# Kernel tuning notes

Hardware: AMD Instinct MI355X
Metric: run time of the kernel (lower is better)

The kernel has to match this reference:

```python
import jax, jax.numpy as jnp
import numpy as np

N, E, G = 8192, 65536, 16          # atoms, edges, graphs in batch
NUM_ELEM, C, NB = 10, 64, 8        # elements, hidden channels, bessel basis
LMAX, NLAYERS = 3, 2
LM = (LMAX + 1) ** 2               # 16 spherical-harmonic components
R_MAX, P_CUT = 5.0, 5
EPS = 1e-9


def spherical_harmonics(u):
    # u: [E,3] unit vectors -> real spherical harmonics l<=3, [E,16]
    x, y, z = u[:, 0], u[:, 1], u[:, 2]
    x2, y2, z2 = x * x, y * y, z * z
    sh = [
        jnp.full_like(x, 0.28209479177387814),
        0.4886025119029199 * y, 0.4886025119029199 * z, 0.4886025119029199 * x,
        1.0925484305920792 * x * y, 1.0925484305920792 * y * z,
        0.31539156525252005 * (3.0 * z2 - 1.0),
        1.0925484305920792 * x * z, 0.5462742152960396 * (x2 - y2),
        0.5900435899266435 * y * (3.0 * x2 - y2), 2.890611442640554 * x * y * z,
        0.4570457994644658 * y * (5.0 * z2 - 1.0),
        0.3731763325901154 * z * (5.0 * z2 - 3.0),
        0.4570457994644658 * x * (5.0 * z2 - 1.0),
        1.445305721320277 * z * (x2 - y2),
        0.5900435899266435 * x * (x2 - 3.0 * y2),
    ]
    return jnp.stack(sh, axis=-1)


def radial_embedding(r):
    # Bessel radial basis with polynomial envelope cutoff -> [E, NB]
    u = r / R_MAX
    p = float(P_CUT)
    cut = (1.0 - 0.5 * (p + 1.0) * (p + 2.0) * u ** P_CUT
           + p * (p + 2.0) * u ** (P_CUT + 1)
           - 0.5 * p * (p + 1.0) * u ** (P_CUT + 2))
    cut = jnp.where(u < 1.0, cut, 0.0)
    n = jnp.arange(1, NB + 1, dtype=r.dtype)
    bessel = jnp.sqrt(2.0 / R_MAX) * jnp.sin(n[None, :] * jnp.pi * u[:, None]) \
             / jnp.maximum(r, EPS)[:, None]
    return bessel * cut[:, None]


def setup_inputs() -> dict:
    key = jax.random.key(0)
    ks = jax.random.split(key, 10)
    positions = jax.random.uniform(ks[0], (N, 3), jnp.float32) * 10.0
    elems = jax.random.randint(ks[1], (N,), 0, NUM_ELEM)
    node_attrs = jax.nn.one_hot(elems, NUM_ELEM, dtype=jnp.float32)
    edge_index = jax.random.randint(ks[2], (2, E), 0, N).astype(jnp.int32)
    shifts = jnp.zeros((E, 3), jnp.float32)
    batch = jnp.sort(jax.random.randint(ks[3], (N,), 0, G)).astype(jnp.int32)
    W_embed = jax.random.normal(ks[4], (NUM_ELEM, C), jnp.float32) / np.sqrt(NUM_ELEM)
    atomic_energies_w = jnp.arange(-1.0, -(NUM_ELEM + 1.0), -1.0, dtype=jnp.float32)
    W_rad = jax.random.normal(ks[5], (NLAYERS, NB, C), jnp.float32) / np.sqrt(NB)
    W_prod = jax.random.normal(ks[6], (NLAYERS, NUM_ELEM, (LMAX + 1) * C, C),
                               jnp.float32) / np.sqrt((LMAX + 1) * C)
    w_read = jax.random.normal(ks[7], (C,), jnp.float32) / np.sqrt(C)
    return {"positions": positions, "node_attrs": node_attrs, "shifts": shifts,
            "W_embed": W_embed, "atomic_energies_w": atomic_energies_w,
            "W_rad": W_rad, "W_prod": W_prod, "w_read": w_read,
            "edge_index": edge_index, "batch": batch}


def _energy(positions, node_attrs, shifts, W_embed, atomic_energies_w,
            W_rad, W_prod, w_read, edge_index, batch):
    snd, rcv = edge_index[0], edge_index[1]
    vec = positions[rcv] - positions[snd] + shifts            # [E,3]
    length = jnp.sqrt(jnp.sum(vec * vec, axis=-1) + EPS)      # [E]
    Y = spherical_harmonics(vec / length[:, None])            # [E,LM]
    R = radial_embedding(length)                              # [E,NB]

    e0 = jax.ops.segment_sum(node_attrs @ atomic_energies_w, batch, num_segments=G)
    h = node_attrs @ W_embed                                  # [N,C]

    for layer in range(NLAYERS):
        w = R @ W_rad[layer]                                  # [E,C] radial weights
        msg = (w * h[snd])[:, None, :] * Y[:, :, None]        # [E,LM,C] tensor product
        A = jax.ops.segment_sum(msg, rcv, num_segments=N)     # [N,LM,C] atomic basis
        A2 = A * A
        # invariant (rotation-invariant) contraction: sum over m within each l
        B = jnp.concatenate(
            [A2[:, l * l:(l + 1) * (l + 1), :].sum(axis=1) for l in range(LMAX + 1)],
            axis=-1)                                          # [N,(LMAX+1)*C]
        # element-dependent product-basis mixing
        h = jnp.einsum('nf,efc,ne->nc', B, W_prod[layer], node_attrs)

    node_e = h @ w_read                                       # [N]
    inter_e = jax.ops.segment_sum(node_e, batch, num_segments=G)
    return e0 + inter_e                                       # [G]


def reference(positions, node_attrs, shifts, W_embed, atomic_energies_w,
              W_rad, W_prod, w_read, edge_index, batch):
    energy = _energy(positions, node_attrs, shifts, W_embed, atomic_energies_w,
                     W_rad, W_prod, w_read, edge_index, batch)
    forces = -jax.grad(
        lambda p: _energy(p, node_attrs, shifts, W_embed, atomic_energies_w,
                          W_rad, W_prod, w_read, edge_index, batch).sum()
    )(positions)
    return energy, forces
```

## Files before the change

kernel.cpp:

```cpp
#include <hip/hip_runtime.h>
#include <math.h>

#define NN 8192
#define NE 65536
#define NG 16
#define NEL 10
#define CC 64
#define NLM 16
#define MAXST 32
#define PI_F 3.14159265358979f

__device__ __forceinline__ int lm_l(int lm) {
    return (lm == 0) ? 0 : (lm < 4) ? 1 : (lm < 9) ? 2 : 3;
}

__device__ __forceinline__ void stage_pack(
    const float* __restrict__ PK, const int* __restrict__ SSND,
    int beg, int cnt, int c, float* sPK, int* sS)
{
    int tot = cnt * 24;
    for (int i = c; i < tot; i += 64) sPK[i] = PK[(size_t)beg*24 + i];
    if (c < cnt) sS[c] = SSND[beg + c];
    __builtin_amdgcn_wave_barrier();
}

__global__ __launch_bounds__(256) void k_front(
    const float* __restrict__ pos, const float* __restrict__ shifts,
    const int* __restrict__ snd, const int* __restrict__ rcv,
    float* __restrict__ Y, float* __restrict__ R,
    float* __restrict__ U, float* __restrict__ L, int* __restrict__ cnt,
    const float* __restrict__ attrs, const float* __restrict__ Wemb,
    const float* __restrict__ aew, const int* __restrict__ batch,
    float* __restrict__ h0, int* __restrict__ elem, int* __restrict__ ecnt,
    float* __restrict__ out,
    const float* __restrict__ Wprod1, const float* __restrict__ wread,
    float* __restrict__ vb1)
{
    __shared__ int hcnt[NEL];
    int bx = blockIdx.x;
    if (bx < 256) {
        int e = bx * 256 + threadIdx.x;
        int s = snd[e], r = rcv[e];
        float vx = pos[r*3+0] - pos[s*3+0] + shifts[e*3+0];
        float vy = pos[r*3+1] - pos[s*3+1] + shifts[e*3+1];
        float vz = pos[r*3+2] - pos[s*3+2] + shifts[e*3+2];
        float len = sqrtf(vx*vx + vy*vy + vz*vz + 1e-9f);
        L[e] = len;
        if (len >= 5.0f) return;
        atomicAdd(&cnt[r], 1);
        float x = vx/len, y = vy/len, z = vz/len;
        U[e*3+0] = x; U[e*3+1] = y; U[e*3+2] = z;
        float x2 = x*x, y2 = y*y, z2 = z*z;
        float4* Yv = (float4*)(Y + (size_t)e*16);
        Yv[0] = make_float4(0.28209479177387814f,
                            0.4886025119029199f*y,
                            0.4886025119029199f*z,
                            0.4886025119029199f*x);
        Yv[1] = make_float4(1.0925484305920792f*x*y,
                            1.0925484305920792f*y*z,
                            0.31539156525252005f*(3.f*z2 - 1.f),
                            1.0925484305920792f*x*z);
        Yv[2] = make_float4(0.5462742152960396f*(x2 - y2),
                            0.5900435899266435f*y*(3.f*x2 - y2),
                            2.890611442640554f*x*y*z,
                            0.4570457994644658f*y*(5.f*z2 - 1.f));
        Yv[3] = make_float4(0.3731763325901154f*z*(5.f*z2 - 3.f),
                            0.4570457994644658f*x*(5.f*z2 - 1.f),
                            1.445305721320277f*z*(x2 - y2),
                            0.5900435899266435f*x*(x2 - 3.f*y2));
        float ur = len * 0.2f;
        float u2 = ur*ur, u4 = u2*u2, u5 = u4*ur, u6 = u5*ur, u7 = u6*ur;
        float cut = 1.f - 21.f*u5 + 35.f*u6 - 15.f*u7;
        const float s2f = 0.632455532033676f;
        float th = (PI_F/5.f) * len;
        float s1, c1; sincosf(th, &s1, &c1);
        float sn_ = s1, cs = c1;
        float coef = s2f * cut / len;
        float rv[8];
#pragma unroll
        for (int nb = 0; nb < 8; nb++) {
            rv[nb] = coef * sn_;
            float ns = sn_*c1 + cs*s1;
            float nc = cs*c1 - sn_*s1;
            sn_ = ns; cs = nc;
        }
        float4* Rv = (float4*)(R + (size_t)e*8);
        Rv[0] = make_float4(rv[0], rv[1], rv[2], rv[3]);
        Rv[1] = make_float4(rv[4], rv[5], rv[6], rv[7]);
    } else if (bx < 768) {
        int t = threadIdx.x, c = t & 63, w = t >> 6;
        if (t < NEL) hcnt[t] = 0;
        __syncthreads();
        float esum = 0.f; int curb = -1;
        for (int g = 0; g < 4; g++) {
            int n = (bx - 256)*16 + w*4 + g;
            float hv = 0.f;
            for (int el = 0; el < NEL; el++) hv += attrs[n*NEL+el] * Wemb[el*CC+c];
            h0[(size_t)n*CC+c] = hv;
            int el = 0; float e0 = 0.f;
            for (int k = 0; k < NEL; k++) {
                float a = attrs[n*NEL+k];
                e0 += a * aew[k];
                if (a > 0.5f) el = k;
            }
            if (c == 0) {
                elem[n] = el;
                atomicAdd(&hcnt[el], 1);
            }
            int b = batch[n];
            if (b != curb) {
                if (curb >= 0 && c == 0) atomicAdd(&out[curb], esum);
                curb = b; esum = 0.f;
            }
            esum += e0;
        }
        if (curb >= 0 && c == 0) atomicAdd(&out[curb], esum);
        __syncthreads();
        if (t < NEL) { int v = hcnt[t]; if (v) atomicAdd(&ecnt[t], v); }
    } else {
        int el = bx - 768, f = threadIdx.x;
        float s = 0.f;
        for (int c = 0; c < CC; c++) s += wread[c] * Wprod1[(size_t)el*256*CC + f*CC + c];
        vb1[el*256+f] = s;
    }
}

__global__ __launch_bounds__(1024) void k_scan(
    const int* __restrict__ cnt, int* __restrict__ offs,
    const int* __restrict__ ecnt, int* __restrict__ eoff)
{
    __shared__ int wsum[16];
    int t = threadIdx.x, lane = t & 63, w = t >> 6;
    int loc[8];
    int run = 0;
#pragma unroll
    for (int i = 0; i < 8; i++) { int v = cnt[t*8+i]; loc[i] = run; run += v; }
    int v = run;
#pragma unroll
    for (int o = 1; o < 64; o <<= 1) {
        int u = __shfl_up(v, o, 64);
        if (lane >= o) v += u;
    }
    if (lane == 63) wsum[w] = v;
    __syncthreads();
    if (t < 16) {
        int x = wsum[t];
#pragma unroll
        for (int o = 1; o < 16; o <<= 1) {
            int u = __shfl_up(x, o, 64);
            if (t >= o) x += u;
        }
        wsum[t] = x;
    }
    __syncthreads();
    int wpre = (w == 0) ? 0 : wsum[w-1];
    int pre = wpre + v - run;
#pragma unroll
    for (int i = 0; i < 8; i++) offs[t*8+i] = pre + loc[i];
    if (t == 1023) offs[NN] = pre + run;
    if (t == 0) {
        int r = 0;
        for (int el = 0; el < NEL; el++) { eoff[el] = r; r += ecnt[el]; }
        eoff[NEL] = r;
    }
}

__global__ void k_scatpack(
    const int* __restrict__ snd, const int* __restrict__ rcv,
    const float* __restrict__ Y, const float* __restrict__ R,
    const float* __restrict__ U, const float* __restrict__ L,
    const int* __restrict__ offs, int* __restrict__ cur,
    float* __restrict__ PK, int* __restrict__ SSND, int* __restrict__ SRCV,
    float* __restrict__ UL,
    const int* __restrict__ elem, const int* __restrict__ eoff,
    int* __restrict__ ecur, int* __restrict__ nbe)
{
    int e = blockIdx.x * blockDim.x + threadIdx.x;
    if (e < NN) {
        int el = elem[e];
        int p = eoff[el] + atomicAdd(&ecur[el], 1);
        nbe[p] = e;
    }
    if (e >= NE) return;
    if (L[e] >= 5.0f) return;
    int r = rcv[e];
    int p = offs[r] + atomicAdd(&cur[r], 1);
    const float4* Yp = (const float4*)(Y + (size_t)e*16);
    float4* d = (float4*)(PK + (size_t)p*24);
    d[0] = Yp[0]; d[1] = Yp[1]; d[2] = Yp[2]; d[3] = Yp[3];
    const float4* Rp = (const float4*)(R + (size_t)e*8);
    d[4] = Rp[0]; d[5] = Rp[1];
    SSND[p] = snd[e];
    SRCV[p] = rcv[e];
    ((float4*)UL)[p] = make_float4(U[e*3+0], U[e*3+1], U[e*3+2], L[e]);
}

__global__ __launch_bounds__(256) void k_fwd0(
    const float* __restrict__ PK, const int* __restrict__ SSND,
    const float* __restrict__ Wrad0, const float* __restrict__ Wprod0,
    const float* __restrict__ h0, const float* __restrict__ attrs,
    const int* __restrict__ elem, const int* __restrict__ offs,
    const int* __restrict__ nbe, float* __restrict__ h1,
    float* __restrict__ A0)
{
    __shared__ __align__(16) float sB[4][1024];
    __shared__ __align__(16) float sPK[4][MAXST*24];
    __shared__ int sS[4][MAXST];
    int t = threadIdx.x, c = t & 63, w = t >> 6;
    float wr[8];
#pragma unroll
    for (int nb = 0; nb < 8; nb++) wr[nb] = Wrad0[nb*CC+c];
    int nid[4], nel[4]; float na[4];
#pragma unroll
    for (int g = 0; g < 4; g++) {
        int n = nbe[blockIdx.x*16 + w*4 + g];
        nid[g] = n;
        int el = elem[n]; nel[g] = el; na[g] = attrs[n*NEL+el];
        float acc[NLM];
#pragma unroll
        for (int lm = 0; lm < NLM; lm++) acc[lm] = 0.f;
        int beg = offs[n], end = offs[n+1];
        for (int base = beg; base < end; base += MAXST) {
            int m = min(MAXST, end - base);
            stage_pack(PK, SSND, base, m, c, sPK[w], sS[w]);
            for (int cb = 0; cb < m; cb += 4) {
                float hb[4];
#pragma unroll
                for (int k = 0; k < 4; k++)
                    hb[k] = (cb+k < m) ? h0[(size_t)sS[w][cb+k]*CC + c] : 0.f;
#pragma unroll
                for (int jj = 0; jj < 4; jj++) {
                    if (cb+jj >= m) break;
                    const float* rec = &sPK[w][(cb+jj)*24];
                    float wv = 0.f;
#pragma unroll
                    for (int nb = 0; nb < 8; nb++) wv += rec[16+nb]*wr[nb];
                    float tt = wv * hb[jj];
#pragma unroll
                    for (int lm = 0; lm < NLM; lm++) acc[lm] += rec[lm]*tt;
                }
            }
            __builtin_amdgcn_wave_barrier();
        }
#pragma unroll
        for (int lm = 0; lm < NLM; lm++) A0[(size_t)n*1024 + lm*64 + c] = acc[lm];
        float b0 = acc[0]*acc[0];
        float b1 = acc[1]*acc[1] + acc[2]*acc[2] + acc[3]*acc[3];
        float b2 = acc[4]*acc[4] + acc[5]*acc[5] + acc[6]*acc[6] + acc[7]*acc[7] + acc[8]*acc[8];
        float b3 = 0.f;
#pragma unroll
        for (int lm = 9; lm < 16; lm++) b3 += acc[lm]*acc[lm];
        sB[w][g*256 + 0*64 + c] = b0;
        sB[w][g*256 + 1*64 + c] = b1;
        sB[w][g*256 + 2*64 + c] = b2;
        sB[w][g*256 + 3*64 + c] = b3;
    }
    __builtin_amdgcn_wave_barrier();
    float hv[4] = {0.f, 0.f, 0.f, 0.f};
    int done = 0;
    while (done != 0xF) {
        int g0 = __ffs(~done & 0xF) - 1;
        int el = (g0==0) ? nel[0] : (g0==1) ? nel[1] : (g0==2) ? nel[2] : nel[3];
        int msk = 0;
#pragma unroll
        for (int g = 0; g < 4; g++) if (nel[g] == el) msk |= 1 << g;
        const float* Wn = Wprod0 + (size_t)el*256*CC;
        float tmp[4] = {0.f, 0.f, 0.f, 0.f};
        for (int f4 = 0; f4 < 64; f4++) {
            float wv0 = Wn[(f4*4+0)*CC + c];
            float wv1 = Wn[(f4*4+1)*CC + c];
            float wv2 = Wn[(f4*4+2)*CC + c];
            float wv3 = Wn[(f4*4+3)*CC + c];
#pragma unroll
            for (int g = 0; g < 4; g++) {
                float4 b = *((const float4*)&sB[w][g*256 + f4*4]);
                tmp[g] += b.x*wv0 + b.y*wv1 + b.z*wv2 + b.w*wv3;
            }
        }
#pragma unroll
        for (int g = 0; g < 4; g++) if ((msk >> g) & 1) hv[g] = tmp[g];
        done |= msk;
    }
#pragma unroll
    for (int g = 0; g < 4; g++) h1[(size_t)nid[g]*CC + c] = na[g]*hv[g];
}

__global__ __launch_bounds__(256) void k_gseed(
    const float* __restrict__ gh1, const float* __restrict__ Wprod0,
    const float* __restrict__ attrs, const int* __restrict__ elem,
    const int* __restrict__ nbe, float* __restrict__ GB)
{
    __shared__ __align__(16) float sgh[4][4][64];
    int t = threadIdx.x, c = t & 63, w = t >> 6;
    int nid[4], nel[4]; float na[4];
#pragma unroll
    for (int g = 0; g < 4; g++) {
        int n = nbe[blockIdx.x*16 + w*4 + g];
        nid[g] = n;
        int el = elem[n]; nel[g] = el; na[g] = attrs[n*NEL+el];
        sgh[w][g][c] = gh1[(size_t)n*CC + c];
    }
    __builtin_amdgcn_wave_barrier();
    float outv[4][4];
    int done = 0;
    while (done != 0xF) {
        int g0 = __ffs(~done & 0xF) - 1;
        int el = (g0==0) ? nel[0] : (g0==1) ? nel[1] : (g0==2) ? nel[2] : nel[3];
        int msk = 0;
#pragma unroll
        for (int g = 0; g < 4; g++) if (nel[g] == el) msk |= 1 << g;
        const float* W0 = Wprod0 + (size_t)el*256*CC;
#pragma unroll
        for (int l = 0; l < 4; l++) {
            const float4* row = (const float4*)(W0 + (size_t)(l*64 + c)*CC);
            float t4[4] = {0.f, 0.f, 0.f, 0.f};
#pragma unroll 4
            for (int k4 = 0; k4 < 16; k4++) {
                float4 wv = row[k4];
#pragma unroll
                for (int g = 0; g < 4; g++) {
                    float4 gg = *((const float4*)&sgh[w][g][k4*4]);
                    t4[g] += wv.x*gg.x + wv.y*gg.y + wv.z*gg.z + wv.w*gg.w;
                }
            }
#pragma unroll
            for (int g = 0; g < 4; g++) if ((msk >> g) & 1) outv[l][g] = t4[g];
        }
        done |= msk;
    }
#pragma unroll
    for (int g = 0; g < 4; g++)
#pragma unroll
        for (int l = 0; l < 4; l++)
            GB[(size_t)nid[g]*256 + l*64 + c] = na[g]*outv[l][g];
}

__global__ __launch_bounds__(256) void k_fbwd(
    const float* __restrict__ PK, const int* __restrict__ SSND,
    const float* __restrict__ Wrad, const float* __restrict__ hprev,
    const float* __restrict__ vb1, const float* __restrict__ GB,
    const float* __restrict__ A0,
    const float* __restrict__ attrs, const int* __restrict__ elem,
    const int* __restrict__ batch, const int* __restrict__ offs,
    float* __restrict__ gYp, float* __restrict__ gRp, float* __restrict__ gh,
    float* __restrict__ out, int layer1)
{
    __shared__ __align__(16) float wrls[8*68];
    __shared__ __align__(16) float sPK[4][MAXST*24];
    __shared__ int sS[4][MAXST];
    __shared__ __align__(16) float Mls[4][16*68];
    __shared__ __align__(16) float Tls[4][4*68];
    __shared__ __align__(16) float Gls[4][4*68];
    int t = threadIdx.x, c = t & 63, w = t >> 6;
    float wr[8];
#pragma unroll
    for (int nb = 0; nb < 8; nb++) wr[nb] = Wrad[nb*CC+c];
    if (w == 0) {
#pragma unroll
        for (int nb = 0; nb < 8; nb++) wrls[nb*68+c] = wr[nb];
    }
    __syncthreads();
    float esum = 0.f; int curb = -1;
    for (int g = 0; g < 4; g++) {
        int n = blockIdx.x*16 + w*4 + g;
        int el = elem[n];
        float a = attrs[n*NEL+el];
        float g4[4];
        if (layer1) {
#pragma unroll
            for (int l = 0; l < 4; l++) g4[l] = a * vb1[el*256 + l*64 + c];
        } else {
#pragma unroll
            for (int l = 0; l < 4; l++) g4[l] = GB[(size_t)n*256 + l*64 + c];
        }
        int beg = offs[n], end = offs[n+1];
        int cnt = end - beg;
        float acc[NLM];
        bool cached = false;
        if (layer1) {
#pragma unroll
            for (int lm = 0; lm < NLM; lm++) acc[lm] = 0.f;
            for (int base = beg; base < end; base += MAXST) {
                int m = min(MAXST, end - base);
                stage_pack(PK, SSND, base, m, c, sPK[w], sS[w]);
                for (int cb = 0; cb < m; cb += 4) {
                    float hb[4];
#pragma unroll
                    for (int k = 0; k < 4; k++)
                        hb[k] = (cb+k < m) ? hprev[(size_t)sS[w][cb+k]*CC + c] : 0.f;
#pragma unroll
                    for (int jj = 0; jj < 4; jj++) {
                        if (cb+jj >= m) break;
                        const float* rec = &sPK[w][(cb+jj)*24];
                        float wv = 0.f;
#pragma unroll
                        for (int nb = 0; nb < 8; nb++) wv += rec[16+nb]*wr[nb];
                        float tt = wv * hb[jj];
#pragma unroll
                        for (int lm = 0; lm < NLM; lm++) acc[lm] += rec[lm]*tt;
                    }
                }
                __builtin_amdgcn_wave_barrier();
            }
            cached = (cnt <= MAXST);
            float b0 = acc[0]*acc[0];
            float b1 = acc[1]*acc[1] + acc[2]*acc[2] + acc[3]*acc[3];
            float b2 = acc[4]*acc[4] + acc[5]*acc[5] + acc[6]*acc[6] + acc[7]*acc[7] + acc[8]*acc[8];
            float b3 = 0.f;
#pragma unroll
            for (int lm = 9; lm < 16; lm++) b3 += acc[lm]*acc[lm];
            float ep = b0*vb1[el*256+c] + b1*vb1[el*256+64+c]
                     + b2*vb1[el*256+128+c] + b3*vb1[el*256+192+c];
#pragma unroll
            for (int o = 32; o > 0; o >>= 1) ep += __shfl_xor(ep, o, 64);
            int b = batch[n];
            if (b != curb) {
                if (curb >= 0 && c == 0) atomicAdd(&out[curb], esum);
                curb = b; esum = 0.f;
            }
            esum += a * ep;
        } else {
#pragma unroll
            for (int lm = 0; lm < NLM; lm++) acc[lm] = A0[(size_t)n*1024 + lm*64 + c];
        }
        float M[NLM];
#pragma unroll
        for (int lm = 0; lm < NLM; lm++) {
            M[lm] = 2.f * acc[lm] * g4[lm_l(lm)];
            Mls[w][lm*68+c] = M[lm];
        }
        __builtin_amdgcn_wave_barrier();
        for (int base = beg; base < end; base += MAXST) {
            int m = min(MAXST, end - base);
            if (!cached) stage_pack(PK, SSND, base, m, c, sPK[w], sS[w]);
            for (int cb = 0; cb < m; cb += 4) {
                int ncq = min(4, m - cb);
                float hb[4];
#pragma unroll
                for (int k = 0; k < 4; k++)
                    hb[k] = (cb+k < m) ? hprev[(size_t)sS[w][cb+k]*CC + c] : 0.f;
#pragma unroll
                for (int jj = 0; jj < 4; jj++) {
                    if (jj >= ncq) break;
                    const float* rec = &sPK[w][(cb+jj)*24];
                    float wv = 0.f;
#pragma unroll
                    for (int nb = 0; nb < 8; nb++) wv += rec[16+nb]*wr[nb];
                    float hvv = hb[jj];
                    float my = 0.f;
#pragma unroll
                    for (int lm = 0; lm < NLM; lm++) my += M[lm]*rec[lm];
                    Tls[w][jj*68+c] = wv * hvv;
                    Gls[w][jj*68+c] = hvv * my;
                    if (layer1) atomicAdd(&gh[(size_t)sS[w][cb+jj]*CC + c], wv * my);
                }
                __builtin_amdgcn_wave_barrier();
                {
                    int jj = c >> 4, lm = c & 15;
                    if (jj < ncq) {
                        const float4* mrow = (const float4*)&Mls[w][lm*68];
                        const float4* trow = (const float4*)&Tls[w][jj*68];
                        float s_ = 0.f;
#pragma unroll
                        for (int k4 = 0; k4 < 16; k4++) {
                            float4 mm = mrow[k4]; float4 tv = trow[k4];
                            s_ += mm.x*tv.x + mm.y*tv.y + mm.z*tv.z + mm.w*tv.w;
                        }
                        size_t p = (size_t)(base + cb + jj);
                        if (layer1) gYp[p*16+lm] = s_;
                        else        gYp[p*16+lm] += s_;
                    }
                }
                if (c < 32) {
                    int jj = c >> 3, nb = c & 7;
                    if (jj < ncq) {
                        const float4* wrow = (const float4*)&wrls[nb*68];
                        const float4* grow = (const float4*)&Gls[w][jj*68];
                        float s_ = 0.f;
#pragma unroll
                        for (int k4 = 0; k4 < 16; k4++) {
                            float4 wv4 = wrow[k4]; float4 gv = grow[k4];
                            s_ += wv4.x*gv.x + wv4.y*gv.y + wv4.z*gv.z + wv4.w*gv.w;
                        }
                        size_t p = (size_t)(base + cb + jj);
                        if (layer1) gRp[p*8+nb] = s_;
                        else        gRp[p*8+nb] += s_;
                    }
                }
                __builtin_amdgcn_wave_barrier();
            }
        }
    }
    if (curb >= 0 && c == 0) atomicAdd(&out[curb], esum);
}

__global__ void k_geo_bwd(const float* __restrict__ gYp, const float* __restrict__ gRp,
                          const float* __restrict__ UL, const int* __restrict__ SSND,
                          const int* __restrict__ SRCV, const int* __restrict__ offs,
                          float* __restrict__ F)
{
    int p = blockIdx.x * blockDim.x + threadIdx.x;
    if (p >= offs[NN]) return;
    float4 ul = ((const float4*)UL)[p];
    float x = ul.x, y = ul.y, z = ul.z, len = ul.w;
    float g[16];
    {
        const float4* gv = (const float4*)(gYp + (size_t)p*16);
        float4 a0 = gv[0], a1 = gv[1], a2 = gv[2], a3 = gv[3];
        g[0]=a0.x; g[1]=a0.y; g[2]=a0.z; g[3]=a0.w;
        g[4]=a1.x; g[5]=a1.y; g[6]=a1.z; g[7]=a1.w;
        g[8]=a2.x; g[9]=a2.y; g[10]=a2.z; g[11]=a2.w;
        g[12]=a3.x; g[13]=a3.y; g[14]=a3.z; g[15]=a3.w;
    }
    float gr[8];
    {
        const float4* rv = (const float4*)(gRp + (size_t)p*8);
        float4 r0 = rv[0], r1 = rv[1];
        gr[0]=r0.x; gr[1]=r0.y; gr[2]=r0.z; gr[3]=r0.w;
        gr[4]=r1.x; gr[5]=r1.y; gr[6]=r1.z; gr[7]=r1.w;
    }
    float x2 = x*x, y2 = y*y, z2 = z*z;
    float gx = 0.f, gy = 0.f, gz = 0.f;
    gx += 0.4886025119029199f*g[3];
    gy += 0.4886025119029199f*g[1];
    gz += 0.4886025119029199f*g[2];
    gx += 1.0925484305920792f*y*g[4];  gy += 1.0925484305920792f*x*g[4];
    gy += 1.0925484305920792f*z*g[5];  gz += 1.0925484305920792f*y*g[5];
    gz += 1.8923493915151203f*z*g[6];
    gx += 1.0925484305920792f*z*g[7];  gz += 1.0925484305920792f*x*g[7];
    gx += 1.0925484305920792f*x*g[8];  gy -= 1.0925484305920792f*y*g[8];
    gx += 3.540261539559861f*x*y*g[9];
    gy += 0.5900435899266435f*(3.f*x2 - 3.f*y2)*g[9];
    gx += 2.890611442640554f*y*z*g[10]; gy += 2.890611442640554f*x*z*g[10]; gz += 2.890611442640554f*x*y*g[10];
    gy += 0.4570457994644658f*(5.f*z2 - 1.f)*g[11]; gz += 4.570457994644658f*y*z*g[11];
    gz += 0.3731763325901154f*(15.f*z2 - 3.f)*g[12];
    gx += 0.4570457994644658f*(5.f*z2 - 1.f)*g[13]; gz += 4.570457994644658f*x*z*g[13];
    gx += 2.890611442640554f*x*z*g[14]; gy -= 2.890611442640554f*y*z*g[14];
    gz += 1.445305721320277f*(x2 - y2)*g[14];
    gx += 0.5900435899266435f*(3.f*x2 - 3.f*y2)*g[15];
    gy -= 3.540261539559861f*x*y*g[15];
    float ur = len * 0.2f;
    float gL = 0.f;
    {
        float u2 = ur*ur, u4 = u2*u2, u5 = u4*ur, u6 = u5*ur, u7 = u6*ur;
        float poly  = 1.f - 21.f*u5 + 35.f*u6 - 15.f*u7;
        float dpoly = (-105.f*u4 + 210.f*u5 - 105.f*u6)*0.2f;
        const float s2f = 0.632455532033676f;
        const float k1 = PI_F/5.f;
        float th = k1*len;
        float s1, c1; sincosf(th, &s1, &c1);
        float sn_ = s1, cs = c1;
        float inv_r = 1.f/len;
        bool tiny = (len < 2e-3f);
#pragma unroll
        for (int nb = 0; nb < 8; nb++) {
            float kn = k1*(float)(nb+1);
            float bes = s2f*sn_*inv_r;
            float dbes;
            if (tiny) dbes = -s2f*kn*kn*kn*len*(1.f/3.f);
            else      dbes = s2f*(kn*cs - sn_*inv_r)*inv_r;
            gL += gr[nb]*(dbes*poly + bes*dpoly);
            float ns = sn_*c1 + cs*s1;
            float nc = cs*c1 - sn_*s1;
            sn_ = ns; cs = nc;
        }
    }
    float dot = gx*x + gy*y + gz*z;
    float gvx = (gx - dot*x)/len + gL*x;
    float gvy = (gy - dot*y)/len + gL*y;
    float gvz = (gz - dot*z)/len + gL*z;
    int sn = SSND[p], rn = SRCV[p];
    atomicAdd(&F[rn*3+0], -gvx);
    atomicAdd(&F[rn*3+1], -gvy);
    atomicAdd(&F[rn*3+2], -gvz);
    atomicAdd(&F[sn*3+0],  gvx);
    atomicAdd(&F[sn*3+1],  gvy);
    atomicAdd(&F[sn*3+2],  gvz);
}

extern "C" void kernel_launch(void* const* d_in, const int* in_sizes, int n_in,
                              void* d_out, int out_size, void* d_ws, size_t ws_size,
                              hipStream_t stream)
{
    const float* positions  = (const float*)d_in[0];
    const float* node_attrs = (const float*)d_in[1];
    const float* shifts     = (const float*)d_in[2];
    const float* W_embed    = (const float*)d_in[3];
    const float* aew        = (const float*)d_in[4];
    const float* W_rad      = (const float*)d_in[5];
    const float* W_prod     = (const float*)d_in[6];
    const float* w_read     = (const float*)d_in[7];
    const int*   edge_index = (const int*)d_in[8];
    const int*   batch      = (const int*)d_in[9];
    float* out = (float*)d_out;

    const int* snd = edge_index;
    const int* rcv = edge_index + NE;

    char* ws = (char*)d_ws;
    size_t off = 0;
    auto allocf = [&](size_t nelems) -> float* {
        float* p = (float*)(ws + off); off += nelems * sizeof(float); return p;
    };
    float* Y    = allocf((size_t)NE*16);
    float* R    = allocf((size_t)NE*8);
    float* U    = allocf((size_t)NE*3);
    float* L    = allocf((size_t)NE);
    float* PK   = allocf((size_t)NE*24);
    float* UL   = allocf((size_t)NE*4);
    float* H0   = allocf((size_t)NN*CC);
    float* H1   = allocf((size_t)NN*CC);
    float* A0   = allocf((size_t)NN*1024);
    float* GYP  = allocf((size_t)NE*16);
    float* GRP  = allocf((size_t)NE*8);
    float* GB   = allocf((size_t)NN*256);
    float* VB1  = allocf((size_t)NEL*256);
    size_t zero_off = off;
    float* GH1  = allocf((size_t)NN*CC);
    int* CNT   = (int*)(ws + off); off += (size_t)NN*4;
    int* CUR   = (int*)(ws + off); off += (size_t)NN*4;
    int* ECNT  = (int*)(ws + off); off += 16*4;
    int* ECUR  = (int*)(ws + off); off += 16*4;
    size_t zero_bytes = off - zero_off;
    int* ELEM  = (int*)(ws + off); off += (size_t)NN*4;
    int* OFFS  = (int*)(ws + off); off += (size_t)(NN+1)*4;
    int* SSND  = (int*)(ws + off); off += (size_t)NE*4;
    int* SRCV  = (int*)(ws + off); off += (size_t)NE*4;
    int* ELOFF = (int*)(ws + off); off += 16*4;
    int* NBE   = (int*)(ws + off); off += (size_t)NN*4;

    hipMemsetAsync(out, 0, (size_t)out_size * sizeof(float), stream);
    hipMemsetAsync(ws + zero_off, 0, zero_bytes, stream);

    const float* Wrad0  = W_rad;
    const float* Wrad1  = W_rad + 8*CC;
    const float* Wprod0 = W_prod;
    const float* Wprod1 = W_prod + (size_t)NEL*256*CC;

    k_front<<<256 + 512 + NEL, 256, 0, stream>>>(
        positions, shifts, snd, rcv, Y, R, U, L, CNT,
        node_attrs, W_embed, aew, batch, H0, ELEM, ECNT, out,
        Wprod1, w_read, VB1);
    k_scan<<<1, 1024, 0, stream>>>(CNT, OFFS, ECNT, ELOFF);
    k_scatpack<<<NE/256, 256, 0, stream>>>(snd, rcv, Y, R, U, L, OFFS, CUR,
                                           PK, SSND, SRCV, UL, ELEM, ELOFF, ECUR, NBE);

    k_fwd0<<<NN/16, 256, 0, stream>>>(PK, SSND, Wrad0, Wprod0, H0, node_attrs, ELEM,
                                      OFFS, NBE, H1, A0);
    k_fbwd<<<NN/16, 256, 0, stream>>>(PK, SSND, Wrad1, H1, VB1, GB, A0, node_attrs, ELEM,
                                      batch, OFFS, GYP, GRP, GH1, out, 1);
    k_gseed<<<NN/16, 256, 0, stream>>>(GH1, Wprod0, node_attrs, ELEM, NBE, GB);
    k_fbwd<<<NN/16, 256, 0, stream>>>(PK, SSND, Wrad0, H0, VB1, GB, A0, node_attrs, ELEM,
                                      batch, OFFS, GYP, GRP, GH1, out, 0);

    k_geo_bwd<<<NE/256, 256, 0, stream>>>(GYP, GRP, UL, SSND, SRCV, OFFS, out + NG);
    (void)in_sizes; (void)n_in; (void)ws_size;
}
```

Baseline: 288.1 us.

## Split fwd0 into accumulate and matvec kernels, one node per wave

The fused layer-0 forward kernel is split into k_acc0, which accumulates the atomic basis with one node per wave and writes the invariant B features to a buffer, and k_matvec0, which does the element-grouped product mixing. k_fbwd is also changed from four nodes per wave to one node per wave, giving four times as many blocks. The LDS staging of packed edge records is removed: records are read directly from global memory and sender indices are made wave-uniform with readfirstlane. This aims for more parallelism and less load imbalance, at the cost of an extra launch and a B0 round trip through memory (reusing the GB buffer). The energy reduction now issues one atomic per node instead of one per graph run, adding atomic traffic.

```diff
diff --git a/kernel.cpp b/kernel.cpp
--- a/kernel.cpp
+++ b/kernel.cpp
@@ -7,22 +7,12 @@
 #define NEL 10
 #define CC 64
 #define NLM 16
-#define MAXST 32
 #define PI_F 3.14159265358979f
 
 __device__ __forceinline__ int lm_l(int lm) {
     return (lm == 0) ? 0 : (lm < 4) ? 1 : (lm < 9) ? 2 : 3;
 }
-
-__device__ __forceinline__ void stage_pack(
-    const float* __restrict__ PK, const int* __restrict__ SSND,
-    int beg, int cnt, int c, float* sPK, int* sS)
-{
-    int tot = cnt * 24;
-    for (int i = c; i < tot; i += 64) sPK[i] = PK[(size_t)beg*24 + i];
-    if (c < cnt) sS[c] = SSND[beg + c];
-    __builtin_amdgcn_wave_barrier();
-}
+__device__ __forceinline__ int rfl(int v) { return __builtin_amdgcn_readfirstlane(v); }
 
 __global__ __launch_bounds__(256) void k_front(
     const float* __restrict__ pos, const float* __restrict__ shifts,
@@ -195,65 +185,70 @@
     ((float4*)UL)[p] = make_float4(U[e*3+0], U[e*3+1], U[e*3+2], L[e]);
 }
 
-__global__ __launch_bounds__(256) void k_fwd0(
+__global__ __launch_bounds__(256) void k_acc0(
     const float* __restrict__ PK, const int* __restrict__ SSND,
-    const float* __restrict__ Wrad0, const float* __restrict__ Wprod0,
-    const float* __restrict__ h0, const float* __restrict__ attrs,
-    const int* __restrict__ elem, const int* __restrict__ offs,
-    const int* __restrict__ nbe, float* __restrict__ h1,
-    float* __restrict__ A0)
+    const float* __restrict__ Wrad0, const float* __restrict__ h0,
+    const int* __restrict__ offs,
+    float* __restrict__ A0, float* __restrict__ B0)
+{
+    int t = threadIdx.x, c = t & 63, w = t >> 6;
+    int n = blockIdx.x*4 + w;
+    float wr[8];
+#pragma unroll
+    for (int nb = 0; nb < 8; nb++) wr[nb] = Wrad0[nb*CC+c];
+    int beg = rfl(offs[n]), end = rfl(offs[n+1]);
+    float acc[NLM];
+#pragma unroll
+    for (int lm = 0; lm < NLM; lm++) acc[lm] = 0.f;
+    for (int p0 = beg; p0 < end; p0 += 4) {
+        int sidx[4]; float hb[4];
+#pragma unroll
+        for (int k = 0; k < 4; k++)
+            sidx[k] = (p0+k < end) ? rfl(SSND[p0+k]) : 0;
+#pragma unroll
+        for (int k = 0; k < 4; k++)
+            hb[k] = (p0+k < end) ? h0[(size_t)sidx[k]*CC + c] : 0.f;
+#pragma unroll
+        for (int jj = 0; jj < 4; jj++) {
+            if (p0+jj >= end) break;
+            const float* rec = PK + (size_t)(p0+jj)*24;
+            float wv = 0.f;
+#pragma unroll
+            for (int nb = 0; nb < 8; nb++) wv += rec[16+nb]*wr[nb];
+            float tt = wv * hb[jj];
+#pragma unroll
+            for (int lm = 0; lm < NLM; lm++) acc[lm] += rec[lm]*tt;
+        }
+    }
+#pragma unroll
+    for (int lm = 0; lm < NLM; lm++) A0[(size_t)n*1024 + lm*64 + c] = acc[lm];
+    float b0 = acc[0]*acc[0];
+    float b1 = acc[1]*acc[1] + acc[2]*acc[2] + acc[3]*acc[3];
+    float b2 = acc[4]*acc[4] + acc[5]*acc[5] + acc[6]*acc[6] + acc[7]*acc[7] + acc[8]*acc[8];
+    float b3 = 0.f;
+#pragma unroll
+    for (int lm = 9; lm < 16; lm++) b3 += acc[lm]*acc[lm];
+    B0[(size_t)n*256 + 0*64 + c] = b0;
+    B0[(size_t)n*256 + 1*64 + c] = b1;
+    B0[(size_t)n*256 + 2*64 + c] = b2;
+    B0[(size_t)n*256 + 3*64 + c] = b3;
+}
+
+__global__ __launch_bounds__(256) void k_matvec0(
+    const float* __restrict__ B0, const float* __restrict__ Wprod0,
+    const float* __restrict__ attrs, const int* __restrict__ elem,
+    const int* __restrict__ nbe, float* __restrict__ h1)
 {
     __shared__ __align__(16) float sB[4][1024];
-    __shared__ __align__(16) float sPK[4][MAXST*24];
-    __shared__ int sS[4][MAXST];
     int t = threadIdx.x, c = t & 63, w = t >> 6;
-    float wr[8];
-#pragma unroll
-    for (int nb = 0; nb < 8; nb++) wr[nb] = Wrad0[nb*CC+c];
     int nid[4], nel[4]; float na[4];
 #pragma unroll
     for (int g = 0; g < 4; g++) {
         int n = nbe[blockIdx.x*16 + w*4 + g];
         nid[g] = n;
         int el = elem[n]; nel[g] = el; na[g] = attrs[n*NEL+el];
-        float acc[NLM];
-#pragma unroll
-        for (int lm = 0; lm < NLM; lm++) acc[lm] = 0.f;
-        int beg = offs[n], end = offs[n+1];
-        for (int base = beg; base < end; base += MAXST) {
-            int m = min(MAXST, end - base);
-            stage_pack(PK, SSND, base, m, c, sPK[w], sS[w]);
-            for (int cb = 0; cb < m; cb += 4) {
-                float hb[4];
-#pragma unroll
-                for (int k = 0; k < 4; k++)
-                    hb[k] = (cb+k < m) ? h0[(size_t)sS[w][cb+k]*CC + c] : 0.f;
-#pragma unroll
-                for (int jj = 0; jj < 4; jj++) {
-                    if (cb+jj >= m) break;
-                    const float* rec = &sPK[w][(cb+jj)*24];
-                    float wv = 0.f;
-#pragma unroll
-                    for (int nb = 0; nb < 8; nb++) wv += rec[16+nb]*wr[nb];
-                    float tt = wv * hb[jj];
-#pragma unroll
-                    for (int lm = 0; lm < NLM; lm++) acc[lm] += rec[lm]*tt;
-                }
-            }
-            __builtin_amdgcn_wave_barrier();
-        }
-#pragma unroll
-        for (int lm = 0; lm < NLM; lm++) A0[(size_t)n*1024 + lm*64 + c] = acc[lm];
-        float b0 = acc[0]*acc[0];
-        float b1 = acc[1]*acc[1] + acc[2]*acc[2] + acc[3]*acc[3];
-        float b2 = acc[4]*acc[4] + acc[5]*acc[5] + acc[6]*acc[6] + acc[7]*acc[7] + acc[8]*acc[8];
-        float b3 = 0.f;
-#pragma unroll
-        for (int lm = 9; lm < 16; lm++) b3 += acc[lm]*acc[lm];
-        sB[w][g*256 + 0*64 + c] = b0;
-        sB[w][g*256 + 1*64 + c] = b1;
-        sB[w][g*256 + 2*64 + c] = b2;
-        sB[w][g*256 + 3*64 + c] = b3;
+#pragma unroll
+        for (int l = 0; l < 4; l++) sB[w][g*256 + l*64 + c] = B0[(size_t)n*256 + l*64 + c];
     }
     __builtin_amdgcn_wave_barrier();
     float hv[4] = {0.f, 0.f, 0.f, 0.f};
@@ -346,12 +341,11 @@
     float* __restrict__ out, int layer1)
 {
     __shared__ __align__(16) float wrls[8*68];
-    __shared__ __align__(16) float sPK[4][MAXST*24];
-    __shared__ int sS[4][MAXST];
     __shared__ __align__(16) float Mls[4][16*68];
     __shared__ __align__(16) float Tls[4][4*68];
     __shared__ __align__(16) float Gls[4][4*68];
     int t = threadIdx.x, c = t & 63, w = t >> 6;
+    int n = blockIdx.x*4 + w;
     float wr[8];
 #pragma unroll
     for (int nb = 0; nb < 8; nb++) wr[nb] = Wrad[nb*CC+c];
@@ -360,138 +354,122 @@
         for (int nb = 0; nb < 8; nb++) wrls[nb*68+c] = wr[nb];
     }
     __syncthreads();
-    float esum = 0.f; int curb = -1;
-    for (int g = 0; g < 4; g++) {
-        int n = blockIdx.x*16 + w*4 + g;
-        int el = elem[n];
-        float a = attrs[n*NEL+el];
-        float g4[4];
-        if (layer1) {
-#pragma unroll
-            for (int l = 0; l < 4; l++) g4[l] = a * vb1[el*256 + l*64 + c];
-        } else {
-#pragma unroll
-            for (int l = 0; l < 4; l++) g4[l] = GB[(size_t)n*256 + l*64 + c];
-        }
-        int beg = offs[n], end = offs[n+1];
-        int cnt = end - beg;
-        float acc[NLM];
-        bool cached = false;
-        if (layer1) {
-#pragma unroll
-            for (int lm = 0; lm < NLM; lm++) acc[lm] = 0.f;
-            for (int base = beg; base < end; base += MAXST) {
-                int m = min(MAXST, end - base);
-                stage_pack(PK, SSND, base, m, c, sPK[w], sS[w]);
-                for (int cb = 0; cb < m; cb += 4) {
-                    float hb[4];
-#pragma unroll
-                    for (int k = 0; k < 4; k++)
-                        hb[k] = (cb+k < m) ? hprev[(size_t)sS[w][cb+k]*CC + c] : 0.f;
-#pragma unroll
-                    for (int jj = 0; jj < 4; jj++) {
-                        if (cb+jj >= m) break;
-                        const float* rec = &sPK[w][(cb+jj)*24];
-                        float wv = 0.f;
-#pragma unroll
-                        for (int nb = 0; nb < 8; nb++) wv += rec[16+nb]*wr[nb];
-                        float tt = wv * hb[jj];
-#pragma unroll
-                        for (int lm = 0; lm < NLM; lm++) acc[lm] += rec[lm]*tt;
-                    }
+    int el = elem[n];
+    float a = attrs[n*NEL+el];
+    float g4[4];
+    if (layer1) {
+#pragma unroll
+        for (int l = 0; l < 4; l++) g4[l] = a * vb1[el*256 + l*64 + c];
+    } else {
+#pragma unroll
+        for (int l = 0; l < 4; l++) g4[l] = GB[(size_t)n*256 + l*64 + c];
+    }
+    int beg = rfl(offs[n]), end = rfl(offs[n+1]);
+    float acc[NLM];
+    if (layer1) {
+#pragma unroll
+        for (int lm = 0; lm < NLM; lm++) acc[lm] = 0.f;
+        for (int p0 = beg; p0 < end; p0 += 4) {
+            int sidx[4]; float hb[4];
+#pragma unroll
+            for (int k = 0; k < 4; k++)
+                sidx[k] = (p0+k < end) ? rfl(SSND[p0+k]) : 0;
+#pragma unroll
+            for (int k = 0; k < 4; k++)
+                hb[k] = (p0+k < end) ? hprev[(size_t)sidx[k]*CC + c] : 0.f;
+#pragma unroll
+            for (int jj = 0; jj < 4; jj++) {
+                if (p0+jj >= end) break;
+                const float* rec = PK + (size_t)(p0+jj)*24;
+                float wv = 0.f;
+#pragma unroll
+                for (int nb = 0; nb < 8; nb++) wv += rec[16+nb]*wr[nb];
+                float tt = wv * hb[jj];
+#pragma unroll
+                for (int lm = 0; lm < NLM; lm++) acc[lm] += rec[lm]*tt;
+            }
+        }
+        float b0 = acc[0]*acc[0];
+        float b1 = acc[1]*acc[1] + acc[2]*acc[2] + acc[3]*acc[3];
+        float b2 = acc[4]*acc[4] + acc[5]*acc[5] + acc[6]*acc[6] + acc[7]*acc[7] + acc[8]*acc[8];
+        float b3 = 0.f;
+#pragma unroll
+        for (int lm = 9; lm < 16; lm++) b3 += acc[lm]*acc[lm];
+        float ep = b0*vb1[el*256+c] + b1*vb1[el*256+64+c]
+                 + b2*vb1[el*256+128+c] + b3*vb1[el*256+192+c];
+#pragma unroll
+        for (int o = 32; o > 0; o >>= 1) ep += __shfl_xor(ep, o, 64);
+        if (c == 0) atomicAdd(&out[batch[n]], a*ep);
+    } else {
+#pragma unroll
+        for (int lm = 0; lm < NLM; lm++) acc[lm] = A0[(size_t)n*1024 + lm*64 + c];
+    }
+    float M[NLM];
+#pragma unroll
+    for (int lm = 0; lm < NLM; lm++) {
+        M[lm] = 2.f * acc[lm] * g4[lm_l(lm)];
+        Mls[w][lm*68+c] = M[lm];
+    }
+    __builtin_amdgcn_wave_barrier();
+    for (int p0 = beg; p0 < end; p0 += 4) {
+        int np = min(4, end - p0);
+        int sidx[4]; float hb[4];
+#pragma unroll
+        for (int k = 0; k < 4; k++)
+            sidx[k] = (p0+k < end) ? rfl(SSND[p0+k]) : 0;
+#pragma unroll
+        for (int k = 0; k < 4; k++)
+            hb[k] = (p0+k < end) ? hprev[(size_t)sidx[k]*CC + c] : 0.f;
+#pragma unroll
+        for (int jj = 0; jj < 4; jj++) {
+            if (jj >= np) break;
+            const float* rec = PK + (size_t)(p0+jj)*24;
+            float wv = 0.f;
+#pragma unroll
+            for (int nb = 0; nb < 8; nb++) wv += rec[16+nb]*wr[nb];
+            float hvv = hb[jj];
+            float my = 0.f;
+#pragma unroll
+            for (int lm = 0; lm < NLM; lm++) my += M[lm]*rec[lm];
+            Tls[w][jj*68+c] = wv * hvv;
+            Gls[w][jj*68+c] = hvv * my;
+            if (layer1) atomicAdd(&gh[(size_t)sidx[jj]*CC + c], wv * my);
+        }
+        __builtin_amdgcn_wave_barrier();
+        {
+            int jj = c >> 4, lm = c & 15;
+            if (jj < np) {
+                const float4* mrow = (const float4*)&Mls[w][lm*68];
+                const float4* trow = (const float4*)&Tls[w][jj*68];
+                float s_ = 0.f;
+#pragma unroll
+                for (int k4 = 0; k4 < 16; k4++) {
+                    float4 mm = mrow[k4]; float4 tv = trow[k4];
+                    s_ += mm.x*tv.x + mm.y*tv.y + mm.z*tv.z + mm.w*tv.w;
                 }
-                __builtin_amdgcn_wave_barrier();
-            }
-            cached = (cnt <= MAXST);
-            float b0 = acc[0]*acc[0];
-            float b1 = acc[1]*acc[1] + acc[2]*acc[2] + acc[3]*acc[3];
-            float b2 = acc[4]*acc[4] + acc[5]*acc[5] + acc[6]*acc[6] + acc[7]*acc[7] + acc[8]*acc[8];
-            float b3 = 0.f;
-#pragma unroll
-            for (int lm = 9; lm < 16; lm++) b3 += acc[lm]*acc[lm];
-            float ep = b0*vb1[el*256+c] + b1*vb1[el*256+64+c]
-                     + b2*vb1[el*256+128+c] + b3*vb1[el*256+192+c];
-#pragma unroll
-            for (int o = 32; o > 0; o >>= 1) ep += __shfl_xor(ep, o, 64);
-            int b = batch[n];
-            if (b != curb) {
-                if (curb >= 0 && c == 0) atomicAdd(&out[curb], esum);
-                curb = b; esum = 0.f;
-            }
-            esum += a * ep;
-        } else {
-#pragma unroll
-            for (int lm = 0; lm < NLM; lm++) acc[lm] = A0[(size_t)n*1024 + lm*64 + c];
-        }
-        float M[NLM];
-#pragma unroll
-        for (int lm = 0; lm < NLM; lm++) {
-            M[lm] = 2.f * acc[lm] * g4[lm_l(lm)];
-            Mls[w][lm*68+c] = M[lm];
+                size_t p = (size_t)(p0 + jj);
+                if (layer1) gYp[p*16+lm] = s_;
+                else        gYp[p*16+lm] += s_;
+            }
+        }
+        if (c < 32) {
+            int jj = c >> 3, nb = c & 7;
+            if (jj < np) {
+                const float4* wrow = (const float4*)&wrls[nb*68];
+                const float4* grow = (const float4*)&Gls[w][jj*68];
+                float s_ = 0.f;
+#pragma unroll
+                for (int k4 = 0; k4 < 16; k4++) {
+                    float4 wv4 = wrow[k4]; float4 gv = grow[k4];
+                    s_ += wv4.x*gv.x + wv4.y*gv.y + wv4.z*gv.z + wv4.w*gv.w;
+                }
+                size_t p = (size_t)(p0 + jj);
+                if (layer1) gRp[p*8+nb] = s_;
+                else        gRp[p*8+nb] += s_;
+            }
         }
         __builtin_amdgcn_wave_barrier();
-        for (int base = beg; base < end; base += MAXST) {
-            int m = min(MAXST, end - base);
-            if (!cached) stage_pack(PK, SSND, base, m, c, sPK[w], sS[w]);
-            for (int cb = 0; cb < m; cb += 4) {
-                int ncq = min(4, m - cb);
-                float hb[4];
-#pragma unroll
-                for (int k = 0; k < 4; k++)
-                    hb[k] = (cb+k < m) ? hprev[(size_t)sS[w][cb+k]*CC + c] : 0.f;
-#pragma unroll
-                for (int jj = 0; jj < 4; jj++) {
-                    if (jj >= ncq) break;
-                    const float* rec = &sPK[w][(cb+jj)*24];
-                    float wv = 0.f;
-#pragma unroll
-                    for (int nb = 0; nb < 8; nb++) wv += rec[16+nb]*wr[nb];
-                    float hvv = hb[jj];
-                    float my = 0.f;
-#pragma unroll
-                    for (int lm = 0; lm < NLM; lm++) my += M[lm]*rec[lm];
-                    Tls[w][jj*68+c] = wv * hvv;
-                    Gls[w][jj*68+c] = hvv * my;
-                    if (layer1) atomicAdd(&gh[(size_t)sS[w][cb+jj]*CC + c], wv * my);
-                }
-                __builtin_amdgcn_wave_barrier();
-                {
-                    int jj = c >> 4, lm = c & 15;
-                    if (jj < ncq) {
-                        const float4* mrow = (const float4*)&Mls[w][lm*68];
-                        const float4* trow = (const float4*)&Tls[w][jj*68];
-                        float s_ = 0.f;
-#pragma unroll
-                        for (int k4 = 0; k4 < 16; k4++) {
-                            float4 mm = mrow[k4]; float4 tv = trow[k4];
-                            s_ += mm.x*tv.x + mm.y*tv.y + mm.z*tv.z + mm.w*tv.w;
-                        }
-                        size_t p = (size_t)(base + cb + jj);
-                        if (layer1) gYp[p*16+lm] = s_;
-                        else        gYp[p*16+lm] += s_;
-                    }
-                }
-                if (c < 32) {
-                    int jj = c >> 3, nb = c & 7;
-                    if (jj < ncq) {
-                        const float4* wrow = (const float4*)&wrls[nb*68];
-                        const float4* grow = (const float4*)&Gls[w][jj*68];
-                        float s_ = 0.f;
-#pragma unroll
-                        for (int k4 = 0; k4 < 16; k4++) {
-                            float4 wv4 = wrow[k4]; float4 gv = grow[k4];
-                            s_ += wv4.x*gv.x + wv4.y*gv.y + wv4.z*gv.z + wv4.w*gv.w;
-                        }
-                        size_t p = (size_t)(base + cb + jj);
-                        if (layer1) gRp[p*8+nb] = s_;
-                        else        gRp[p*8+nb] += s_;
-                    }
-                }
-                __builtin_amdgcn_wave_barrier();
-            }
-        }
-    }
-    if (curb >= 0 && c == 0) atomicAdd(&out[curb], esum);
+    }
 }
 
 __global__ void k_geo_bwd(const float* __restrict__ gYp, const float* __restrict__ gRp,
@@ -645,13 +623,13 @@
     k_scatpack<<<NE/256, 256, 0, stream>>>(snd, rcv, Y, R, U, L, OFFS, CUR,
                                            PK, SSND, SRCV, UL, ELEM, ELOFF, ECUR, NBE);
 
-    k_fwd0<<<NN/16, 256, 0, stream>>>(PK, SSND, Wrad0, Wprod0, H0, node_attrs, ELEM,
-                                      OFFS, NBE, H1, A0);
-    k_fbwd<<<NN/16, 256, 0, stream>>>(PK, SSND, Wrad1, H1, VB1, GB, A0, node_attrs, ELEM,
-                                      batch, OFFS, GYP, GRP, GH1, out, 1);
+    k_acc0<<<NN/4, 256, 0, stream>>>(PK, SSND, Wrad0, H0, OFFS, A0, GB );
+    k_matvec0<<<NN/16, 256, 0, stream>>>(GB , Wprod0, node_attrs, ELEM, NBE, H1);
+    k_fbwd<<<NN/4, 256, 0, stream>>>(PK, SSND, Wrad1, H1, VB1, GB, A0, node_attrs, ELEM,
+                                     batch, OFFS, GYP, GRP, GH1, out, 1);
     k_gseed<<<NN/16, 256, 0, stream>>>(GH1, Wprod0, node_attrs, ELEM, NBE, GB);
-    k_fbwd<<<NN/16, 256, 0, stream>>>(PK, SSND, Wrad0, H0, VB1, GB, A0, node_attrs, ELEM,
-                                      batch, OFFS, GYP, GRP, GH1, out, 0);
+    k_fbwd<<<NN/4, 256, 0, stream>>>(PK, SSND, Wrad0, H0, VB1, GB, A0, node_attrs, ELEM,
+                                     batch, OFFS, GYP, GRP, GH1, out, 0);
 
     k_geo_bwd<<<NE/256, 256, 0, stream>>>(GYP, GRP, UL, SSND, SRCV, OFFS, out + NG);
     (void)in_sizes; (void)n_in; (void)ws_size;
```

Result: slower. 337.4 us (+17.1%).
